# Performance work log

Measured on AMD Instinct MI355X. Metric: run time of the kernel, lower is better.

The kernel has to match this reference:

```python
import jax, jax.numpy as jnp
import numpy as np

B, H, S, D = 4, 16, 2048, 64


def setup_inputs() -> dict:
    key = jax.random.key(0)
    kq, kk, kv = jax.random.split(key, 3)
    q = jax.random.normal(kq, (B, H, S, D), dtype=jnp.float32)
    k = jax.random.normal(kk, (B, H, S, D), dtype=jnp.float32)
    v = jax.random.normal(kv, (B, H, S, D), dtype=jnp.float32)
    # causal mask: 1 where position is masked (j > i), matching mask * -1e9 additive convention
    mask = jnp.triu(jnp.ones((S, S), dtype=jnp.float32), k=1)[None, None]  # [1,1,S,S]
    return {"q": q, "k": k, "v": v, "mask": mask}


def reference(q, k, v, mask):
    scale = 1.0 / jnp.sqrt(jnp.asarray(q.shape[-1], dtype=q.dtype))
    # [B,H,S,S] scores
    scores = jnp.einsum('bhqd,bhkd->bhqk', q, k) * scale
    scores = scores + mask * (-1e9)
    attn = jax.nn.softmax(scores, axis=-1)
    return jnp.einsum('bhqk,bhkd->bhqd', attn, v)
```

## Files before the change

kernel.cpp:

```cpp
#include <hip/hip_runtime.h>
#include <hip/hip_bf16.h>

namespace {

constexpr int Bc = 4, Hc = 16, Sc = 2048, Dc = 64;

using bf16x2 = __attribute__((ext_vector_type(2))) __bf16;
using bf16x8 = __attribute__((ext_vector_type(8))) __bf16;
using f32x4  = __attribute__((ext_vector_type(4))) float;
using f32x16 = __attribute__((ext_vector_type(16))) float;
using uint2v = __attribute__((ext_vector_type(2))) unsigned int;
using uint4v = __attribute__((ext_vector_type(4))) unsigned int;

__device__ __forceinline__ float exp2_hw(float x) {
#if __has_builtin(__builtin_amdgcn_exp2f)
  return __builtin_amdgcn_exp2f(x);
#else
  return exp2f(x);
#endif
}

__device__ __forceinline__ unsigned pk_bf16(float a, float b) {
  bf16x2 t = { (__bf16)a, (__bf16)b };
  return __builtin_bit_cast(unsigned, t);
}

__device__ __forceinline__ void pl32swap(unsigned& a, unsigned& b) {
  asm volatile("s_nop 1\n\tv_permlane32_swap_b32 %0, %1\n\ts_nop 1"
               : "+v"(a), "+v"(b));
}
__device__ __forceinline__ void xhalf_pair(float x, float& lo, float& hi) {
  unsigned a, b;
  asm volatile("v_mov_b32 %0, %2\n\t"
               "v_mov_b32 %1, %2\n\t"
               "s_nop 1\n\t"
               "v_permlane32_swap_b32 %0, %1\n\t"
               "s_nop 1"
               : "=&v"(a), "=&v"(b)
               : "v"(x));
  lo = __builtin_bit_cast(float, a);
  hi = __builtin_bit_cast(float, b);
}
__device__ __forceinline__ float xhalf_sum(float x) {
  float lo, hi; xhalf_pair(x, lo, hi); return lo + hi;
}

__device__ __forceinline__ int vswz(int d) { return ((d >> 4) ^ d) & 7; }

__global__ __launch_bounds__(256, 2)
void fattn_kernel(const float* __restrict__ Q, const float* __restrict__ K,
                  const float* __restrict__ V, float* __restrict__ O) {
  const int tid  = threadIdx.x;
  const int wid  = tid >> 6;
  const int lane = tid & 63;
  const int l31  = lane & 31;
  const int hi   = lane >> 5;

  const int flat = blockIdx.x + 8 * blockIdx.y;
  const int w    = (flat & 7) * 64 + (flat >> 3);
  const int p    = w & 7;
  const int bh   = w >> 3;

  const size_t base = (size_t)bh * (Sc * Dc);
  const float* Qb = Q + base;
  const float* Kb = K + base;
  const float* Vb = V + base;
  float*       Ob = O + base;

  __shared__ __align__(16) __bf16 k_lds[3][64][64];
  __shared__ __align__(16) __bf16 vt_lds[3][64][64];

  const int srow = tid >> 2;
  const int scol = (tid & 3) * 16;
  const int ssw  = (srow & 7) << 3;
  const int vk0  = (tid >> 4) * 4;
  const int vd0  = (tid & 15) * 4;

  constexpr float QSC = 0.125f * 1.44269504088896f;

  f32x4 Rk0, Rk1, Rk2, Rk3, Rv0, Rv1, Rv2, Rv3;

  auto issue_loads = [&](int krow) {
    const float* ksrc = Kb + (size_t)(krow + srow) * Dc + scol;
    Rk0 = *(const f32x4*)ksrc;
    Rk1 = *(const f32x4*)(ksrc + 4);
    Rk2 = *(const f32x4*)(ksrc + 8);
    Rk3 = *(const f32x4*)(ksrc + 12);
    const float* vsrc = Vb + (size_t)(krow + vk0) * Dc + vd0;
    Rv0 = *(const f32x4*)vsrc;
    Rv1 = *(const f32x4*)(vsrc + Dc);
    Rv2 = *(const f32x4*)(vsrc + 2 * Dc);
    Rv3 = *(const f32x4*)(vsrc + 3 * Dc);
  };
  auto write_stage = [&](__bf16 (*kd)[64], __bf16 (*vd)[64]) {
    uint4v w0, w1;
    w0[0] = pk_bf16(Rk0[0], Rk0[1]); w0[1] = pk_bf16(Rk0[2], Rk0[3]);
    w0[2] = pk_bf16(Rk1[0], Rk1[1]); w0[3] = pk_bf16(Rk1[2], Rk1[3]);
    w1[0] = pk_bf16(Rk2[0], Rk2[1]); w1[1] = pk_bf16(Rk2[2], Rk2[3]);
    w1[2] = pk_bf16(Rk3[0], Rk3[1]); w1[3] = pk_bf16(Rk3[2], Rk3[3]);
    *(uint4v*)&kd[srow][scol ^ ssw]       = w0;
    *(uint4v*)&kd[srow][(scol + 8) ^ ssw] = w1;
    #pragma unroll
    for (int e = 0; e < 4; ++e) {
      const int d = vd0 + e;
      uint2v wv2;
      wv2[0] = pk_bf16(Rv0[e], Rv1[e]);
      wv2[1] = pk_bf16(Rv2[e], Rv3[e]);
      *(uint2v*)&vd[d][vk0 ^ (vswz(d) << 3)] = wv2;
    }
  };

  for (int half = 0; half < 2; ++half) {
    const int qp = half ? (15 - p) : p;
    const int qb = qp * 128;
    const int wq = qb + wid * 32;
    const int nkb = 2 * qp + 2;

    bf16x8 qf[4];
    {
      const float* qrow = Qb + (size_t)(wq + l31) * Dc;
      #pragma unroll
      for (int s = 0; s < 4; ++s) {
        const float* src = qrow + s * 16 + hi * 8;
        f32x4 a0 = *(const f32x4*)src;
        f32x4 a1 = *(const f32x4*)(src + 4);
        uint4v wv;
        wv[0] = pk_bf16(a0[0] * QSC, a0[1] * QSC);
        wv[1] = pk_bf16(a0[2] * QSC, a0[3] * QSC);
        wv[2] = pk_bf16(a1[0] * QSC, a1[1] * QSC);
        wv[3] = pk_bf16(a1[2] * QSC, a1[3] * QSC);
        qf[s] = __builtin_bit_cast(bf16x8, wv);
      }
    }

    f32x16 o0, o1;
    #pragma unroll
    for (int i = 0; i < 16; ++i) { o0[i] = 0.f; o1[i] = 0.f; }
    float l = 0.f;

    issue_loads(0);
    write_stage(k_lds[0], vt_lds[0]);
    issue_loads(64);
    __syncthreads();

    for (int t = 0; t < nkb; ++t) {
      const int bq = t % 3;
      const int bw = (t + 1) % 3;
      const int kbase = t * 64;

      if (t + 1 < nkb) write_stage(k_lds[bw], vt_lds[bw]);

      if (t + 2 < nkb) issue_loads((t + 2) * 64);

      asm volatile("s_waitcnt lgkmcnt(0)" ::: "memory");
      __builtin_amdgcn_s_barrier();

      if (kbase <= wq + 31) {
        const __bf16 (*kc)[64] = k_lds[bq];
        const __bf16 (*vc)[64] = vt_lds[bq];

        f32x16 s0, s1;
        #pragma unroll
        for (int i = 0; i < 16; ++i) { s0[i] = 0.f; s1[i] = 0.f; }
        const int ksw = (l31 & 7) << 3;
        __builtin_amdgcn_s_setprio(1);
        #pragma unroll
        for (int s = 0; s < 4; ++s) {
          bf16x8 kf = *(const bf16x8*)&kc[l31][(s * 16 + hi * 8) ^ ksw];
          s0 = __builtin_amdgcn_mfma_f32_32x32x16_bf16(kf, qf[s], s0, 0, 0, 0);
        }
        #pragma unroll
        for (int s = 0; s < 4; ++s) {
          bf16x8 kf = *(const bf16x8*)&kc[32 + l31][(s * 16 + hi * 8) ^ ksw];
          s1 = __builtin_amdgcn_mfma_f32_32x32x16_bf16(kf, qf[s], s1, 0, 0, 0);
        }
        __builtin_amdgcn_s_setprio(0);

        if (kbase + 63 > wq) {
          const int q   = wq + l31;
          const int dq0 = q - (kbase + 4 * hi);
          const int dq1 = q - (kbase + 32 + 4 * hi);
          #pragma unroll
          for (int i = 0; i < 16; ++i) {
            const int off = (i & 3) + 8 * (i >> 2);
            if (off > dq0) s0[i] = -1e30f;
            if (off > dq1) s1[i] = -1e30f;
          }
        }

        #pragma unroll
        for (int i = 0; i < 16; ++i) {
          s0[i] = exp2_hw(s0[i]);
          s1[i] = exp2_hw(s1[i]);
        }
        float sm[16];
        #pragma unroll
        for (int i = 0; i < 16; ++i) sm[i] = s0[i] + s1[i];
        #pragma unroll
        for (int st = 8; st > 0; st >>= 1)
          #pragma unroll
          for (int i = 0; i < st; ++i) sm[i] += sm[i + st];
        l += xhalf_sum(sm[0]);

        uint4v wv;
        unsigned t0, t1, t2, t3;
        t0 = pk_bf16(s0[0], s0[1]);  t1 = pk_bf16(s0[2], s0[3]);
        t2 = pk_bf16(s0[4], s0[5]);  t3 = pk_bf16(s0[6], s0[7]);
        pl32swap(t0, t2); pl32swap(t1, t3);
        wv[0] = t0; wv[1] = t1; wv[2] = t2; wv[3] = t3;
        const bf16x8 pf0 = __builtin_bit_cast(bf16x8, wv);
        t0 = pk_bf16(s0[8], s0[9]);   t1 = pk_bf16(s0[10], s0[11]);
        t2 = pk_bf16(s0[12], s0[13]); t3 = pk_bf16(s0[14], s0[15]);
        pl32swap(t0, t2); pl32swap(t1, t3);
        wv[0] = t0; wv[1] = t1; wv[2] = t2; wv[3] = t3;
        const bf16x8 pf1 = __builtin_bit_cast(bf16x8, wv);
        t0 = pk_bf16(s1[0], s1[1]);  t1 = pk_bf16(s1[2], s1[3]);
        t2 = pk_bf16(s1[4], s1[5]);  t3 = pk_bf16(s1[6], s1[7]);
        pl32swap(t0, t2); pl32swap(t1, t3);
        wv[0] = t0; wv[1] = t1; wv[2] = t2; wv[3] = t3;
        const bf16x8 pf2 = __builtin_bit_cast(bf16x8, wv);
        t0 = pk_bf16(s1[8], s1[9]);   t1 = pk_bf16(s1[10], s1[11]);
        t2 = pk_bf16(s1[12], s1[13]); t3 = pk_bf16(s1[14], s1[15]);
        pl32swap(t0, t2); pl32swap(t1, t3);
        wv[0] = t0; wv[1] = t1; wv[2] = t2; wv[3] = t3;
        const bf16x8 pf3 = __builtin_bit_cast(bf16x8, wv);

        const int vd0c = l31, vd1c = 32 + l31;
        const int vs0 = vswz(vd0c) << 3, vs1 = vswz(vd1c) << 3;
        bf16x8 vf;
        __builtin_amdgcn_s_setprio(1);
        vf = *(const bf16x8*)&vc[vd0c][(hi * 8) ^ vs0];
        o0 = __builtin_amdgcn_mfma_f32_32x32x16_bf16(vf, pf0, o0, 0, 0, 0);
        vf = *(const bf16x8*)&vc[vd0c][(16 + hi * 8) ^ vs0];
        o0 = __builtin_amdgcn_mfma_f32_32x32x16_bf16(vf, pf1, o0, 0, 0, 0);
        vf = *(const bf16x8*)&vc[vd0c][(32 + hi * 8) ^ vs0];
        o0 = __builtin_amdgcn_mfma_f32_32x32x16_bf16(vf, pf2, o0, 0, 0, 0);
        vf = *(const bf16x8*)&vc[vd0c][(48 + hi * 8) ^ vs0];
        o0 = __builtin_amdgcn_mfma_f32_32x32x16_bf16(vf, pf3, o0, 0, 0, 0);
        vf = *(const bf16x8*)&vc[vd1c][(hi * 8) ^ vs1];
        o1 = __builtin_amdgcn_mfma_f32_32x32x16_bf16(vf, pf0, o1, 0, 0, 0);
        vf = *(const bf16x8*)&vc[vd1c][(16 + hi * 8) ^ vs1];
        o1 = __builtin_amdgcn_mfma_f32_32x32x16_bf16(vf, pf1, o1, 0, 0, 0);
        vf = *(const bf16x8*)&vc[vd1c][(32 + hi * 8) ^ vs1];
        o1 = __builtin_amdgcn_mfma_f32_32x32x16_bf16(vf, pf2, o1, 0, 0, 0);
        vf = *(const bf16x8*)&vc[vd1c][(48 + hi * 8) ^ vs1];
        o1 = __builtin_amdgcn_mfma_f32_32x32x16_bf16(vf, pf3, o1, 0, 0, 0);
        __builtin_amdgcn_s_setprio(0);
      }
    }

    const float inv = 1.0f / l;
    float* orow = Ob + (size_t)(wq + l31) * Dc;
    #pragma unroll
    for (int b = 0; b < 4; ++b) {
      f32x4 u0, u1;
      #pragma unroll
      for (int e = 0; e < 4; ++e) { u0[e] = o0[4 * b + e] * inv; u1[e] = o1[4 * b + e] * inv; }
      *(f32x4*)(orow + 8 * b + 4 * hi)      = u0;
      *(f32x4*)(orow + 32 + 8 * b + 4 * hi) = u1;
    }
    __syncthreads();
  }
}

}

extern "C" void kernel_launch(void* const* d_in, const int* in_sizes, int n_in,
                              void* d_out, int out_size, void* d_ws, size_t ws_size,
                              hipStream_t stream) {
  const float* q = (const float*)d_in[0];
  const float* k = (const float*)d_in[1];
  const float* v = (const float*)d_in[2];
  float* o = (float*)d_out;
  dim3 grid(8, Bc * Hc);
  fattn_kernel<<<grid, dim3(256), 0, stream>>>(q, k, v, o);
}
```

Measured before the change: 60.25 us.

## Use 256-row query tiles per block with two 32-row groups per wave

Each block now owns one 256-row query tile, and each wave handles 64 query rows split into two 32-row groups. The old scheme had each block walk two 128-row tiles paired for causal balance. Every staged K/V tile in LDS now feeds twice as many MFMAs, which halves the K/V global reloads and the bf16 conversion and staging work per query row. The 1D grid is remapped so each XCD owns fixed heads and gets balanced short and long tiles, and occupancy is pinned through waves_per_eu. In exchange, registers per wave roughly double (four output accumulators and two Q fragment sets), which risks spills. Causal work is also coarser per block, so load imbalance can grow.

Measured after the change: 69.53 us. 1.15x slower.

```diff
diff --git a/kernel.cpp b/kernel.cpp
--- a/kernel.cpp
+++ b/kernel.cpp
@@ -47,7 +47,8 @@
 
 __device__ __forceinline__ int vswz(int d) { return ((d >> 4) ^ d) & 7; }
 
-__global__ __launch_bounds__(256, 2)
+__global__ __launch_bounds__(256)
+__attribute__((amdgpu_waves_per_eu(2, 2)))
 void fattn_kernel(const float* __restrict__ Q, const float* __restrict__ K,
                   const float* __restrict__ V, float* __restrict__ O) {
   const int tid  = threadIdx.x;
@@ -56,10 +57,19 @@
   const int l31  = lane & 31;
   const int hi   = lane >> 5;
 
-  const int flat = blockIdx.x + 8 * blockIdx.y;
-  const int w    = (flat & 7) * 64 + (flat >> 3);
-  const int p    = w & 7;
-  const int bh   = w >> 3;
+  const int d    = blockIdx.x;
+  const int xcd  = d & 7;
+  const int n    = d >> 3;
+  const int j    = n >> 5;
+  const int ci   = n & 31;
+  const int bh_l = ci & 7;
+  const int b    = ci >> 3;
+  const int P    = j ? b : (7 - b);
+  const int bh   = xcd * 8 + bh_l;
+
+  const int qb  = P * 256;
+  const int wq  = qb + wid * 64;
+  const int nkb = 4 * P + 4;
 
   const size_t base = (size_t)bh * (Sc * Dc);
   const float* Qb = Q + base;
@@ -102,164 +112,178 @@
     *(uint4v*)&kd[srow][(scol + 8) ^ ssw] = w1;
     #pragma unroll
     for (int e = 0; e < 4; ++e) {
-      const int d = vd0 + e;
+      const int dd = vd0 + e;
       uint2v wv2;
       wv2[0] = pk_bf16(Rv0[e], Rv1[e]);
       wv2[1] = pk_bf16(Rv2[e], Rv3[e]);
-      *(uint2v*)&vd[d][vk0 ^ (vswz(d) << 3)] = wv2;
+      *(uint2v*)&vd[dd][vk0 ^ (vswz(dd) << 3)] = wv2;
     }
   };
 
-  for (int half = 0; half < 2; ++half) {
-    const int qp = half ? (15 - p) : p;
-    const int qb = qp * 128;
-    const int wq = qb + wid * 32;
-    const int nkb = 2 * qp + 2;
-
-    bf16x8 qf[4];
-    {
-      const float* qrow = Qb + (size_t)(wq + l31) * Dc;
+  bf16x8 qfA[4], qfB[4];
+  #pragma unroll
+  for (int g = 0; g < 2; ++g) {
+    const float* qrow = Qb + (size_t)(wq + g * 32 + l31) * Dc;
+    #pragma unroll
+    for (int s = 0; s < 4; ++s) {
+      const float* src = qrow + s * 16 + hi * 8;
+      f32x4 a0 = *(const f32x4*)src;
+      f32x4 a1 = *(const f32x4*)(src + 4);
+      uint4v wv;
+      wv[0] = pk_bf16(a0[0] * QSC, a0[1] * QSC);
+      wv[1] = pk_bf16(a0[2] * QSC, a0[3] * QSC);
+      wv[2] = pk_bf16(a1[0] * QSC, a1[1] * QSC);
+      wv[3] = pk_bf16(a1[2] * QSC, a1[3] * QSC);
+      if (g == 0) qfA[s] = __builtin_bit_cast(bf16x8, wv);
+      else        qfB[s] = __builtin_bit_cast(bf16x8, wv);
+    }
+  }
+
+  f32x16 oA0, oA1, oB0, oB1;
+  #pragma unroll
+  for (int i = 0; i < 16; ++i) { oA0[i] = 0.f; oA1[i] = 0.f; oB0[i] = 0.f; oB1[i] = 0.f; }
+  float lA = 0.f, lB = 0.f;
+
+  auto compute_group = [&](int kbase, const __bf16 (*kc)[64], const __bf16 (*vc)[64],
+                           const bf16x8 (&qf)[4], f32x16& o0, f32x16& o1,
+                           float& l, int qg) {
+    f32x16 s0, s1;
+    #pragma unroll
+    for (int i = 0; i < 16; ++i) { s0[i] = 0.f; s1[i] = 0.f; }
+    const int ksw = (l31 & 7) << 3;
+    __builtin_amdgcn_s_setprio(1);
+    #pragma unroll
+    for (int s = 0; s < 4; ++s) {
+      bf16x8 kf = *(const bf16x8*)&kc[l31][(s * 16 + hi * 8) ^ ksw];
+      s0 = __builtin_amdgcn_mfma_f32_32x32x16_bf16(kf, qf[s], s0, 0, 0, 0);
+    }
+    #pragma unroll
+    for (int s = 0; s < 4; ++s) {
+      bf16x8 kf = *(const bf16x8*)&kc[32 + l31][(s * 16 + hi * 8) ^ ksw];
+      s1 = __builtin_amdgcn_mfma_f32_32x32x16_bf16(kf, qf[s], s1, 0, 0, 0);
+    }
+    __builtin_amdgcn_s_setprio(0);
+
+    if (kbase + 63 > qg) {
+      const int q   = qg + l31;
+      const int dq0 = q - (kbase + 4 * hi);
+      const int dq1 = q - (kbase + 32 + 4 * hi);
       #pragma unroll
-      for (int s = 0; s < 4; ++s) {
-        const float* src = qrow + s * 16 + hi * 8;
-        f32x4 a0 = *(const f32x4*)src;
-        f32x4 a1 = *(const f32x4*)(src + 4);
-        uint4v wv;
-        wv[0] = pk_bf16(a0[0] * QSC, a0[1] * QSC);
-        wv[1] = pk_bf16(a0[2] * QSC, a0[3] * QSC);
-        wv[2] = pk_bf16(a1[0] * QSC, a1[1] * QSC);
-        wv[3] = pk_bf16(a1[2] * QSC, a1[3] * QSC);
-        qf[s] = __builtin_bit_cast(bf16x8, wv);
+      for (int i = 0; i < 16; ++i) {
+        const int off = (i & 3) + 8 * (i >> 2);
+        if (off > dq0) s0[i] = -1e30f;
+        if (off > dq1) s1[i] = -1e30f;
       }
     }
 
-    f32x16 o0, o1;
-    #pragma unroll
-    for (int i = 0; i < 16; ++i) { o0[i] = 0.f; o1[i] = 0.f; }
-    float l = 0.f;
-
-    issue_loads(0);
-    write_stage(k_lds[0], vt_lds[0]);
-    issue_loads(64);
-    __syncthreads();
-
-    for (int t = 0; t < nkb; ++t) {
-      const int bq = t % 3;
-      const int bw = (t + 1) % 3;
-      const int kbase = t * 64;
-
-      if (t + 1 < nkb) write_stage(k_lds[bw], vt_lds[bw]);
-
-      if (t + 2 < nkb) issue_loads((t + 2) * 64);
-
-      asm volatile("s_waitcnt lgkmcnt(0)" ::: "memory");
-      __builtin_amdgcn_s_barrier();
-
-      if (kbase <= wq + 31) {
-        const __bf16 (*kc)[64] = k_lds[bq];
-        const __bf16 (*vc)[64] = vt_lds[bq];
-
-        f32x16 s0, s1;
-        #pragma unroll
-        for (int i = 0; i < 16; ++i) { s0[i] = 0.f; s1[i] = 0.f; }
-        const int ksw = (l31 & 7) << 3;
-        __builtin_amdgcn_s_setprio(1);
-        #pragma unroll
-        for (int s = 0; s < 4; ++s) {
-          bf16x8 kf = *(const bf16x8*)&kc[l31][(s * 16 + hi * 8) ^ ksw];
-          s0 = __builtin_amdgcn_mfma_f32_32x32x16_bf16(kf, qf[s], s0, 0, 0, 0);
-        }
-        #pragma unroll
-        for (int s = 0; s < 4; ++s) {
-          bf16x8 kf = *(const bf16x8*)&kc[32 + l31][(s * 16 + hi * 8) ^ ksw];
-          s1 = __builtin_amdgcn_mfma_f32_32x32x16_bf16(kf, qf[s], s1, 0, 0, 0);
-        }
-        __builtin_amdgcn_s_setprio(0);
-
-        if (kbase + 63 > wq) {
-          const int q   = wq + l31;
-          const int dq0 = q - (kbase + 4 * hi);
-          const int dq1 = q - (kbase + 32 + 4 * hi);
-          #pragma unroll
-          for (int i = 0; i < 16; ++i) {
-            const int off = (i & 3) + 8 * (i >> 2);
-            if (off > dq0) s0[i] = -1e30f;
-            if (off > dq1) s1[i] = -1e30f;
-          }
-        }
-
-        #pragma unroll
-        for (int i = 0; i < 16; ++i) {
-          s0[i] = exp2_hw(s0[i]);
-          s1[i] = exp2_hw(s1[i]);
-        }
-        float sm[16];
-        #pragma unroll
-        for (int i = 0; i < 16; ++i) sm[i] = s0[i] + s1[i];
-        #pragma unroll
-        for (int st = 8; st > 0; st >>= 1)
-          #pragma unroll
-          for (int i = 0; i < st; ++i) sm[i] += sm[i + st];
-        l += xhalf_sum(sm[0]);
-
-        uint4v wv;
-        unsigned t0, t1, t2, t3;
-        t0 = pk_bf16(s0[0], s0[1]);  t1 = pk_bf16(s0[2], s0[3]);
-        t2 = pk_bf16(s0[4], s0[5]);  t3 = pk_bf16(s0[6], s0[7]);
-        pl32swap(t0, t2); pl32swap(t1, t3);
-        wv[0] = t0; wv[1] = t1; wv[2] = t2; wv[3] = t3;
-        const bf16x8 pf0 = __builtin_bit_cast(bf16x8, wv);
-        t0 = pk_bf16(s0[8], s0[9]);   t1 = pk_bf16(s0[10], s0[11]);
-        t2 = pk_bf16(s0[12], s0[13]); t3 = pk_bf16(s0[14], s0[15]);
-        pl32swap(t0, t2); pl32swap(t1, t3);
-        wv[0] = t0; wv[1] = t1; wv[2] = t2; wv[3] = t3;
-        const bf16x8 pf1 = __builtin_bit_cast(bf16x8, wv);
-        t0 = pk_bf16(s1[0], s1[1]);  t1 = pk_bf16(s1[2], s1[3]);
-        t2 = pk_bf16(s1[4], s1[5]);  t3 = pk_bf16(s1[6], s1[7]);
-        pl32swap(t0, t2); pl32swap(t1, t3);
-        wv[0] = t0; wv[1] = t1; wv[2] = t2; wv[3] = t3;
-        const bf16x8 pf2 = __builtin_bit_cast(bf16x8, wv);
-        t0 = pk_bf16(s1[8], s1[9]);   t1 = pk_bf16(s1[10], s1[11]);
-        t2 = pk_bf16(s1[12], s1[13]); t3 = pk_bf16(s1[14], s1[15]);
-        pl32swap(t0, t2); pl32swap(t1, t3);
-        wv[0] = t0; wv[1] = t1; wv[2] = t2; wv[3] = t3;
-        const bf16x8 pf3 = __builtin_bit_cast(bf16x8, wv);
-
-        const int vd0c = l31, vd1c = 32 + l31;
-        const int vs0 = vswz(vd0c) << 3, vs1 = vswz(vd1c) << 3;
-        bf16x8 vf;
-        __builtin_amdgcn_s_setprio(1);
-        vf = *(const bf16x8*)&vc[vd0c][(hi * 8) ^ vs0];
-        o0 = __builtin_amdgcn_mfma_f32_32x32x16_bf16(vf, pf0, o0, 0, 0, 0);
-        vf = *(const bf16x8*)&vc[vd0c][(16 + hi * 8) ^ vs0];
-        o0 = __builtin_amdgcn_mfma_f32_32x32x16_bf16(vf, pf1, o0, 0, 0, 0);
-        vf = *(const bf16x8*)&vc[vd0c][(32 + hi * 8) ^ vs0];
-        o0 = __builtin_amdgcn_mfma_f32_32x32x16_bf16(vf, pf2, o0, 0, 0, 0);
-        vf = *(const bf16x8*)&vc[vd0c][(48 + hi * 8) ^ vs0];
-        o0 = __builtin_amdgcn_mfma_f32_32x32x16_bf16(vf, pf3, o0, 0, 0, 0);
-        vf = *(const bf16x8*)&vc[vd1c][(hi * 8) ^ vs1];
-        o1 = __builtin_amdgcn_mfma_f32_32x32x16_bf16(vf, pf0, o1, 0, 0, 0);
-        vf = *(const bf16x8*)&vc[vd1c][(16 + hi * 8) ^ vs1];
-        o1 = __builtin_amdgcn_mfma_f32_32x32x16_bf16(vf, pf1, o1, 0, 0, 0);
-        vf = *(const bf16x8*)&vc[vd1c][(32 + hi * 8) ^ vs1];
-        o1 = __builtin_amdgcn_mfma_f32_32x32x16_bf16(vf, pf2, o1, 0, 0, 0);
-        vf = *(const bf16x8*)&vc[vd1c][(48 + hi * 8) ^ vs1];
-        o1 = __builtin_amdgcn_mfma_f32_32x32x16_bf16(vf, pf3, o1, 0, 0, 0);
-        __builtin_amdgcn_s_setprio(0);
-      }
-    }
-
-    const float inv = 1.0f / l;
+    #pragma unroll
+    for (int i = 0; i < 16; ++i) {
+      s0[i] = exp2_hw(s0[i]);
+      s1[i] = exp2_hw(s1[i]);
+    }
+    float sm[16];
+    #pragma unroll
+    for (int i = 0; i < 16; ++i) sm[i] = s0[i] + s1[i];
+    #pragma unroll
+    for (int st = 8; st > 0; st >>= 1)
+      #pragma unroll
+      for (int i = 0; i < st; ++i) sm[i] += sm[i + st];
+    l += xhalf_sum(sm[0]);
+
+    uint4v wv;
+    unsigned t0, t1, t2, t3;
+    t0 = pk_bf16(s0[0], s0[1]);  t1 = pk_bf16(s0[2], s0[3]);
+    t2 = pk_bf16(s0[4], s0[5]);  t3 = pk_bf16(s0[6], s0[7]);
+    pl32swap(t0, t2); pl32swap(t1, t3);
+    wv[0] = t0; wv[1] = t1; wv[2] = t2; wv[3] = t3;
+    const bf16x8 pf0 = __builtin_bit_cast(bf16x8, wv);
+    t0 = pk_bf16(s0[8], s0[9]);   t1 = pk_bf16(s0[10], s0[11]);
+    t2 = pk_bf16(s0[12], s0[13]); t3 = pk_bf16(s0[14], s0[15]);
+    pl32swap(t0, t2); pl32swap(t1, t3);
+    wv[0] = t0; wv[1] = t1; wv[2] = t2; wv[3] = t3;
+    const bf16x8 pf1 = __builtin_bit_cast(bf16x8, wv);
+    t0 = pk_bf16(s1[0], s1[1]);  t1 = pk_bf16(s1[2], s1[3]);
+    t2 = pk_bf16(s1[4], s1[5]);  t3 = pk_bf16(s1[6], s1[7]);
+    pl32swap(t0, t2); pl32swap(t1, t3);
+    wv[0] = t0; wv[1] = t1; wv[2] = t2; wv[3] = t3;
+    const bf16x8 pf2 = __builtin_bit_cast(bf16x8, wv);
+    t0 = pk_bf16(s1[8], s1[9]);   t1 = pk_bf16(s1[10], s1[11]);
+    t2 = pk_bf16(s1[12], s1[13]); t3 = pk_bf16(s1[14], s1[15]);
+    pl32swap(t0, t2); pl32swap(t1, t3);
+    wv[0] = t0; wv[1] = t1; wv[2] = t2; wv[3] = t3;
+    const bf16x8 pf3 = __builtin_bit_cast(bf16x8, wv);
+
+    const int vc0 = l31, vc1 = 32 + l31;
+    const int vs0 = vswz(vc0) << 3, vs1 = vswz(vc1) << 3;
+    bf16x8 vf;
+    __builtin_amdgcn_s_setprio(1);
+    vf = *(const bf16x8*)&vc[vc0][(hi * 8) ^ vs0];
+    o0 = __builtin_amdgcn_mfma_f32_32x32x16_bf16(vf, pf0, o0, 0, 0, 0);
+    vf = *(const bf16x8*)&vc[vc0][(16 + hi * 8) ^ vs0];
+    o0 = __builtin_amdgcn_mfma_f32_32x32x16_bf16(vf, pf1, o0, 0, 0, 0);
+    vf = *(const bf16x8*)&vc[vc0][(32 + hi * 8) ^ vs0];
+    o0 = __builtin_amdgcn_mfma_f32_32x32x16_bf16(vf, pf2, o0, 0, 0, 0);
+    vf = *(const bf16x8*)&vc[vc0][(48 + hi * 8) ^ vs0];
+    o0 = __builtin_amdgcn_mfma_f32_32x32x16_bf16(vf, pf3, o0, 0, 0, 0);
+    vf = *(const bf16x8*)&vc[vc1][(hi * 8) ^ vs1];
+    o1 = __builtin_amdgcn_mfma_f32_32x32x16_bf16(vf, pf0, o1, 0, 0, 0);
+    vf = *(const bf16x8*)&vc[vc1][(16 + hi * 8) ^ vs1];
+    o1 = __builtin_amdgcn_mfma_f32_32x32x16_bf16(vf, pf1, o1, 0, 0, 0);
+    vf = *(const bf16x8*)&vc[vc1][(32 + hi * 8) ^ vs1];
+    o1 = __builtin_amdgcn_mfma_f32_32x32x16_bf16(vf, pf2, o1, 0, 0, 0);
+    vf = *(const bf16x8*)&vc[vc1][(48 + hi * 8) ^ vs1];
+    o1 = __builtin_amdgcn_mfma_f32_32x32x16_bf16(vf, pf3, o1, 0, 0, 0);
+    __builtin_amdgcn_s_setprio(0);
+  };
+
+  issue_loads(0);
+  write_stage(k_lds[0], vt_lds[0]);
+  issue_loads(64);
+  __syncthreads();
+
+  for (int t = 0; t < nkb; ++t) {
+    const int bq = t % 3;
+    const int bw = (t + 1) % 3;
+    const int kbase = t * 64;
+
+    if (t + 1 < nkb) write_stage(k_lds[bw], vt_lds[bw]);
+
+    if (t + 2 < nkb) issue_loads((t + 2) * 64);
+
+    asm volatile("s_waitcnt lgkmcnt(0)" ::: "memory");
+    __builtin_amdgcn_s_barrier();
+
+    if (kbase <= wq + 63) {
+      const __bf16 (*kc)[64] = k_lds[bq];
+      const __bf16 (*vc)[64] = vt_lds[bq];
+      compute_group(kbase, kc, vc, qfA, oA0, oA1, lA, wq);
+      compute_group(kbase, kc, vc, qfB, oB0, oB1, lB, wq + 32);
+    }
+  }
+
+  {
+    const float inv = 1.0f / lA;
     float* orow = Ob + (size_t)(wq + l31) * Dc;
     #pragma unroll
-    for (int b = 0; b < 4; ++b) {
+    for (int b2 = 0; b2 < 4; ++b2) {
       f32x4 u0, u1;
       #pragma unroll
-      for (int e = 0; e < 4; ++e) { u0[e] = o0[4 * b + e] * inv; u1[e] = o1[4 * b + e] * inv; }
-      *(f32x4*)(orow + 8 * b + 4 * hi)      = u0;
-      *(f32x4*)(orow + 32 + 8 * b + 4 * hi) = u1;
-    }
-    __syncthreads();
+      for (int e = 0; e < 4; ++e) { u0[e] = oA0[4 * b2 + e] * inv; u1[e] = oA1[4 * b2 + e] * inv; }
+      *(f32x4*)(orow + 8 * b2 + 4 * hi)      = u0;
+      *(f32x4*)(orow + 32 + 8 * b2 + 4 * hi) = u1;
+    }
+  }
+  {
+    const float inv = 1.0f / lB;
+    float* orow = Ob + (size_t)(wq + 32 + l31) * Dc;
+    #pragma unroll
+    for (int b2 = 0; b2 < 4; ++b2) {
+      f32x4 u0, u1;
+      #pragma unroll
+      for (int e = 0; e < 4; ++e) { u0[e] = oB0[4 * b2 + e] * inv; u1[e] = oB1[4 * b2 + e] * inv; }
+      *(f32x4*)(orow + 8 * b2 + 4 * hi)      = u0;
+      *(f32x4*)(orow + 32 + 8 * b2 + 4 * hi) = u1;
+    }
   }
 }
 
@@ -272,6 +296,5 @@
   const float* k = (const float*)d_in[1];
   const float* v = (const float*)d_in[2];
   float* o = (float*)d_out;
-  dim3 grid(8, Bc * Hc);
-  fattn_kernel<<<grid, dim3(256), 0, stream>>>(q, k, v, o);
-}
+  fattn_kernel<<<dim3(512), dim3(256), 0, stream>>>(q, k, v, o);
+}
```
